# Kernel optimization log

Measured on AMD Instinct MI355X. Metric: run time of the kernel, lower is better.

The kernel has to match this reference:

```python
import jax, jax.numpy as jnp
import numpy as np

BN_EPS = 1e-5

def _bn_eval(x, g, b, m, v):
    # BatchNorm1d in eval mode with running stats
    return (x - m) * (g / jnp.sqrt(v + BN_EPS)) + b

def _gcn_layer(x, adj, w, b):
    # D^-0.5 A D^-0.5 (X W) + b  (same math as diag(d^-0.5) @ adj @ diag(d^-0.5))
    deg = adj.sum(axis=1)
    dis = deg ** -0.5
    xw = x @ w
    return dis[:, None] * (adj @ (dis[:, None] * xw)) + b

def setup_inputs() -> dict:
    key = jax.random.key(0)
    ks = jax.random.split(key, 8)
    N, F, E, H, G, C = 16384, 1024, 256, 256, 128, 10
    def xavier(k, i, o):
        s = float(np.sqrt(6.0 / (i + o)))
        return jax.random.uniform(k, (i, o), jnp.float32, -s, s)
    return {
        "feature": jax.random.uniform(ks[0], (N, F), jnp.float32),
        "adj": jax.random.uniform(ks[1], (N, N), jnp.float32),
        "enc_w1": xavier(ks[2], F, 512), "enc_b1": jnp.zeros((512,), jnp.float32),
        "bn1_g": jnp.ones((512,), jnp.float32), "bn1_b": jnp.zeros((512,), jnp.float32),
        "bn1_m": jnp.zeros((512,), jnp.float32), "bn1_v": jnp.ones((512,), jnp.float32),
        "enc_w2": xavier(ks[3], 512, E), "enc_b2": jnp.zeros((E,), jnp.float32),
        "bn2_g": jnp.ones((E,), jnp.float32), "bn2_b": jnp.zeros((E,), jnp.float32),
        "bn2_m": jnp.zeros((E,), jnp.float32), "bn2_v": jnp.ones((E,), jnp.float32),
        "gcn1_w": xavier(ks[4], E, H), "gcn1_b": jnp.zeros((H,), jnp.float32),
        "gcn2_w": xavier(ks[5], H, G), "gcn2_b": jnp.zeros((G,), jnp.float32),
        "cls_w": xavier(ks[6], G, C), "cls_b": jnp.zeros((C,), jnp.float32),
    }

def reference(feature, adj, enc_w1, enc_b1, bn1_g, bn1_b, bn1_m, bn1_v,
              enc_w2, enc_b2, bn2_g, bn2_b, bn2_m, bn2_v,
              gcn1_w, gcn1_b, gcn2_w, gcn2_b, cls_w, cls_b):
    # encoder.encode (eval: dropout off, BN running stats)
    h = jax.nn.relu(_bn_eval(feature @ enc_w1 + enc_b1, bn1_g, bn1_b, bn1_m, bn1_v))
    h = jax.nn.relu(_bn_eval(h @ enc_w2 + enc_b2, bn2_g, bn2_b, bn2_m, bn2_v))
    h = jax.nn.relu(_gcn_layer(h, adj, gcn1_w, gcn1_b))
    h = jax.nn.relu(_gcn_layer(h, adj, gcn2_w, gcn2_b))
    out = jax.nn.sigmoid(h @ cls_w + cls_b)
    return jnp.clip(out, 1e-10, 1 - 1e-10)
```

## Files before the change

### kernel.cpp

```cpp
#include <hip/hip_runtime.h>
#include <stdint.h>

typedef unsigned short u16;
typedef unsigned int u32;
typedef __attribute__((ext_vector_type(4))) float f32x4;
typedef __attribute__((ext_vector_type(16))) float f32x16;
typedef __attribute__((ext_vector_type(8))) short s16x8;
typedef __attribute__((ext_vector_type(4))) short s16x4;
typedef __attribute__((ext_vector_type(2))) unsigned int u32x2;
typedef __attribute__((ext_vector_type(4))) unsigned int u32x4;
typedef __attribute__((ext_vector_type(8))) int i32x8;

__device__ __forceinline__ u16 f2bf(float x){
  unsigned u = __builtin_bit_cast(unsigned, x);
  u += 0x7fffu + ((u >> 16) & 1u);
  return (u16)(u >> 16);
}
__device__ __forceinline__ float bf2f(u16 b){
  return __builtin_bit_cast(float, (unsigned)b << 16);
}
__device__ __forceinline__ u32 pk_fp8x4(float a, float b, float c, float d){
  int w = 0;
  w = __builtin_amdgcn_cvt_pk_fp8_f32(a, b, w, false);
  w = __builtin_amdgcn_cvt_pk_fp8_f32(c, d, w, true);
  return (u32)w;
}


__device__ __forceinline__ void tcvtT_dev(const float* __restrict__ src, u16* __restrict__ dst,
                                          int K, int N, int bx, int by, char* smem){
  float (*t)[33] = (float (*)[33])smem;
  int tx = threadIdx.x & 31, ty = threadIdx.x >> 5;
  int n0 = bx * 32, k0 = by * 32;
  #pragma unroll
  for (int i = 0; i < 4; i++)
    t[ty + 8 * i][tx] = src[(size_t)(k0 + ty + 8 * i) * N + n0 + tx];
  __syncthreads();
  #pragma unroll
  for (int i = 0; i < 4; i++)
    dst[(size_t)(n0 + ty + 8 * i) * K + k0 + tx] = f2bf(t[tx][ty + 8 * i]);
}

__device__ __forceinline__ void bn_dev(const float* __restrict__ g, const float* __restrict__ b,
                                       const float* __restrict__ m, const float* __restrict__ v,
                                       const float* __restrict__ lin_b,
                                       float* __restrict__ s, float* __restrict__ bb,
                                       int n, int blk){
  int i = blk * 256 + threadIdx.x;
  if (i < n){
    float sc = g[i] * rsqrtf(v[i] + 1e-5f);
    s[i] = sc;
    bb[i] = (lin_b[i] - m[i]) * sc + b[i];
  }
}

__global__ __launch_bounds__(256) void prep0_kernel(
    const float* __restrict__ enc_w1, u16* __restrict__ w1t,
    const float* __restrict__ g, const float* __restrict__ b,
    const float* __restrict__ m, const float* __restrict__ v,
    const float* __restrict__ lin_b, float* __restrict__ s1, float* __restrict__ bb1)
{
  __shared__ char smem[32 * 33 * 4 + 64];
  if (blockIdx.x < 512)
    tcvtT_dev(enc_w1, w1t, 1024, 512, blockIdx.x & 15, blockIdx.x >> 4, smem);
  else
    bn_dev(g, b, m, v, lin_b, s1, bb1, 512, blockIdx.x - 512);
}

__global__ __launch_bounds__(256) void enc1_deg_kernel(
    const float* __restrict__ feature, const u16* __restrict__ w1t,
    u16* __restrict__ h1, const float* __restrict__ cs, const float* __restrict__ cb,
    const float* __restrict__ adj, unsigned char* __restrict__ adj8,
    float* __restrict__ dis,
    const float* __restrict__ enc_w2, u16* __restrict__ w2t,
    const float* __restrict__ gcn1_w, u16* __restrict__ g1t,
    const float* __restrict__ gcn2_w, u16* __restrict__ g2t,
    const float* __restrict__ bn2_g, const float* __restrict__ bn2_b,
    const float* __restrict__ bn2_m, const float* __restrict__ bn2_v,
    const float* __restrict__ enc_b2, float* __restrict__ s2, float* __restrict__ bb2)
{
  constexpr int BM = 128, BN = 256, BK = 64, WM = 2, WN = 2;
  constexpr int N = 512, K = 1024, NADJ = 16384;
  constexpr int WTM = BM / WM, WTN = BN / WN, FM = WTM / 16, FN = WTN / 16;
  constexpr int AIT = (BM * BK) / (256 * 4);
  constexpr int BIT = (BN * BK) / (256 * 8);

  __shared__ __align__(16) char smem[BM * BK * 2 + BN * BK * 2];

  if (blockIdx.x >= 16640){
    int p = blockIdx.x - 16640;
    if (p < 128)       tcvtT_dev(enc_w2, w2t, 512, 256, p & 7, p >> 3, smem);
    else if (p < 192){ int l = p - 128; tcvtT_dev(gcn1_w, g1t, 256, 256, l & 7, l >> 3, smem); }
    else if (p < 224){ int l = p - 192; tcvtT_dev(gcn2_w, g2t, 256, 128, l & 3, l >> 2, smem); }
    else               bn_dev(bn2_g, bn2_b, bn2_m, bn2_v, enc_b2, s2, bb2, 256, 0);
    return;
  }

  if (blockIdx.x >= 256){
    int row = blockIdx.x - 256;
    const float* rp = adj + (size_t)row * NADJ;
    unsigned char* wp = adj8 + (size_t)row * NADJ;
    float s = 0.f;
    #pragma unroll
    for (int it = 0; it < 4; ++it){
      const float* p = rp + it * 4096 + threadIdx.x * 16;
      f32x4 v[4];
      #pragma unroll
      for (int j = 0; j < 4; ++j) v[j] = *(const f32x4*)(p + 4 * j);
      u32x4 o;
      #pragma unroll
      for (int j = 0; j < 4; ++j){
        s += (v[j][0] + v[j][1]) + (v[j][2] + v[j][3]);
        o[j] = pk_fp8x4(v[j][0], v[j][1], v[j][2], v[j][3]);
      }
      *(u32x4*)(wp + it * 4096 + threadIdx.x * 16) = o;
    }
    #pragma unroll
    for (int d = 32; d > 0; d >>= 1) s += __shfl_down(s, d, 64);
    float* ps = (float*)smem;
    if ((threadIdx.x & 63) == 0) ps[threadIdx.x >> 6] = s;
    __syncthreads();
    if (threadIdx.x == 0) dis[row] = rsqrtf((ps[0] + ps[1]) + (ps[2] + ps[3]));
    return;
  }

  u16* As = (u16*)smem;
  u16* Bs = (u16*)(smem + BM * BK * 2);
  const int tid = threadIdx.x;
  const int lane = tid & 63;
  const int wid = tid >> 6;
  const int wr = wid / WN;
  const int wc = wid % WN;
  const int bm = (blockIdx.x & 127) * BM;
  const int bn = (blockIdx.x >> 7) * BN;

  f32x4 arf[AIT];
  s16x8 brb[BIT];

  auto load_tiles = [&](int k0){
    #pragma unroll
    for (int i = 0; i < AIT; i++){
      int e = (i * 256 + tid) * 4; int r = e / BK, c = e % BK;
      arf[i] = *(const f32x4*)(feature + (size_t)(bm + r) * K + k0 + c);
    }
    #pragma unroll
    for (int i = 0; i < BIT; i++){
      int e = (i * 256 + tid) * 8; int r = e / BK, c = e % BK;
      brb[i] = *(const s16x8*)(w1t + (size_t)(bn + r) * K + k0 + c);
    }
  };
  auto store_tiles = [&](){
    char* Ac = (char*)As; char* Bc = (char*)Bs;
    #pragma unroll
    for (int i = 0; i < AIT; i++){
      int e = (i * 256 + tid) * 4; int r = e / BK, c = e % BK;
      int off = ((r * BK + c) * 2) ^ ((r & 7) << 4);
      s16x4 o;
      o[0] = (short)f2bf(arf[i][0]); o[1] = (short)f2bf(arf[i][1]);
      o[2] = (short)f2bf(arf[i][2]); o[3] = (short)f2bf(arf[i][3]);
      *(s16x4*)(Ac + off) = o;
    }
    #pragma unroll
    for (int i = 0; i < BIT; i++){
      int e = (i * 256 + tid) * 8; int r = e / BK, c = e % BK;
      int off = ((r * BK + c) * 2) ^ ((r & 7) << 4);
      *(s16x8*)(Bc + off) = brb[i];
    }
  };

  f32x4 acc[FM][FN];
  #pragma unroll
  for (int m = 0; m < FM; m++)
    #pragma unroll
    for (int n = 0; n < FN; n++)
      acc[m][n] = (f32x4){0.f, 0.f, 0.f, 0.f};

  const int arow0 = wr * WTM + (lane & 15);
  const int brow0 = wc * WTN + (lane & 15);
  const int kof = (lane >> 4) * 8;

  load_tiles(0);
  for (int kt = 0; kt < K / BK; ++kt){
    __syncthreads();
    store_tiles();
    __syncthreads();
    if (kt + 1 < K / BK) load_tiles((kt + 1) * BK);
    const char* Ac = (const char*)As;
    const char* Bc = (const char*)Bs;
    #pragma unroll
    for (int ks = 0; ks < BK / 32; ++ks){
      s16x8 af[FM], bfr[FN];
      #pragma unroll
      for (int m = 0; m < FM; m++){
        int r = arow0 + m * 16;
        af[m] = *(const s16x8*)(Ac + (((r * BK + ks * 32 + kof) * 2) ^ ((r & 7) << 4)));
      }
      #pragma unroll
      for (int n = 0; n < FN; n++){
        int r = brow0 + n * 16;
        bfr[n] = *(const s16x8*)(Bc + (((r * BK + ks * 32 + kof) * 2) ^ ((r & 7) << 4)));
      }
      #pragma unroll
      for (int m = 0; m < FM; m++)
        #pragma unroll
        for (int n = 0; n < FN; n++)
          acc[m][n] = __builtin_amdgcn_mfma_f32_16x16x32_bf16(af[m], bfr[n], acc[m][n], 0, 0, 0);
    }
  }
  #pragma unroll
  for (int m = 0; m < FM; m++){
    #pragma unroll
    for (int n = 0; n < FN; n++){
      int col = bn + wc * WTN + n * 16 + (lane & 15);
      int row0 = bm + wr * WTM + m * 16 + (lane >> 4) * 4;
      #pragma unroll
      for (int r4 = 0; r4 < 4; r4++){
        float vv = fmaxf(acc[m][n][r4] * cs[col] + cb[col], 0.f);
        h1[(size_t)(row0 + r4) * N + col] = f2bf(vv);
      }
    }
  }
}

__global__ __launch_bounds__(256, 1)
void h2tT_kernel(const u16* __restrict__ h1, const u16* __restrict__ w2t,
                 const float* __restrict__ s2, const float* __restrict__ bb2,
                 const u16* __restrict__ g1t, const float* __restrict__ dis,
                 unsigned char* __restrict__ tT)
{
  constexpr int M = 16384, K1 = 512, E = 256, K2 = 256, BK = 64;
  constexpr float SC = 256.f;

  __shared__ u16 As[64 * BK];
  __shared__ u16 Bs[256 * BK];
  __shared__ u16 H2s[64 * 256];

  const int tid = threadIdx.x;
  const int lane = tid & 63;
  const int wc = tid >> 6;
  const int bm = blockIdx.x * 64;
  const int arow0 = lane & 15;
  const int kof = (lane >> 4) * 8;

  {
    s16x8 arb[2], brb[8];
    auto load1 = [&](int k0){
      #pragma unroll
      for (int i = 0; i < 2; i++){
        int e = (i * 256 + tid) * 8; int r = e >> 6, c = e & 63;
        arb[i] = *(const s16x8*)(h1 + (size_t)(bm + r) * K1 + k0 + c);
      }
      #pragma unroll
      for (int i = 0; i < 8; i++){
        int e = (i * 256 + tid) * 8; int r = e >> 6, c = e & 63;
        brb[i] = *(const s16x8*)(w2t + (size_t)r * K1 + k0 + c);
      }
    };
    auto store1 = [&](){
      char* Ac = (char*)As; char* Bc = (char*)Bs;
      #pragma unroll
      for (int i = 0; i < 2; i++){
        int e = (i * 256 + tid) * 8; int r = e >> 6, c = e & 63;
        *(s16x8*)(Ac + (((r * BK + c) * 2) ^ ((r & 7) << 4))) = arb[i];
      }
      #pragma unroll
      for (int i = 0; i < 8; i++){
        int e = (i * 256 + tid) * 8; int r = e >> 6, c = e & 63;
        *(s16x8*)(Bc + (((r * BK + c) * 2) ^ ((r & 7) << 4))) = brb[i];
      }
    };

    f32x4 acc[4][4];
    #pragma unroll
    for (int m = 0; m < 4; m++)
      #pragma unroll
      for (int n = 0; n < 4; n++)
        acc[m][n] = (f32x4){0.f, 0.f, 0.f, 0.f};

    load1(0);
    for (int kt = 0; kt < K1 / BK; ++kt){
      __syncthreads();
      store1();
      __syncthreads();
      if (kt + 1 < K1 / BK) load1((kt + 1) * BK);
      const char* Ac = (const char*)As;
      const char* Bc = (const char*)Bs;
      #pragma unroll
      for (int ks = 0; ks < 2; ++ks){
        s16x8 af[4], bfr[4];
        #pragma unroll
        for (int m = 0; m < 4; m++){
          int r = arow0 + m * 16;
          af[m] = *(const s16x8*)(Ac + (((r * BK + ks * 32 + kof) * 2) ^ ((r & 7) << 4)));
        }
        #pragma unroll
        for (int n = 0; n < 4; n++){
          int r = wc * 64 + n * 16 + (lane & 15);
          bfr[n] = *(const s16x8*)(Bc + (((r * BK + ks * 32 + kof) * 2) ^ ((r & 7) << 4)));
        }
        #pragma unroll
        for (int m = 0; m < 4; m++)
          #pragma unroll
          for (int n = 0; n < 4; n++)
            acc[m][n] = __builtin_amdgcn_mfma_f32_16x16x32_bf16(af[m], bfr[n], acc[m][n], 0, 0, 0);
      }
    }
    __syncthreads();
    char* Hc = (char*)H2s;
    #pragma unroll
    for (int m = 0; m < 4; m++){
      #pragma unroll
      for (int n = 0; n < 4; n++){
        int col = wc * 64 + n * 16 + (lane & 15);
        int row0 = m * 16 + (lane >> 4) * 4;
        #pragma unroll
        for (int r4 = 0; r4 < 4; r4++){
          int row = row0 + r4;
          float vv = fmaxf(acc[m][n][r4] * s2[col] + bb2[col], 0.f);
          *(u16*)(Hc + (((row * 256 + col) * 2) ^ ((row & 7) << 4))) = f2bf(vv);
        }
      }
    }
  }

  {
    s16x8 brb[8];
    auto load2 = [&](int k0){
      #pragma unroll
      for (int i = 0; i < 8; i++){
        int e = (i * 256 + tid) * 8; int r = e >> 6, c = e & 63;
        brb[i] = *(const s16x8*)(g1t + (size_t)r * K2 + k0 + c);
      }
    };
    auto store2 = [&](){
      char* Bc = (char*)Bs;
      #pragma unroll
      for (int i = 0; i < 8; i++){
        int e = (i * 256 + tid) * 8; int r = e >> 6, c = e & 63;
        *(s16x8*)(Bc + (((r * BK + c) * 2) ^ ((r & 7) << 4))) = brb[i];
      }
    };

    f32x4 acc[4][4];
    #pragma unroll
    for (int m = 0; m < 4; m++)
      #pragma unroll
      for (int n = 0; n < 4; n++)
        acc[m][n] = (f32x4){0.f, 0.f, 0.f, 0.f};

    load2(0);
    for (int kt = 0; kt < K2 / BK; ++kt){
      __syncthreads();
      store2();
      __syncthreads();
      if (kt + 1 < K2 / BK) load2((kt + 1) * BK);
      const char* Hc = (const char*)H2s;
      const char* Bc = (const char*)Bs;
      #pragma unroll
      for (int ks = 0; ks < 2; ++ks){
        s16x8 af[4], bfr[4];
        #pragma unroll
        for (int m = 0; m < 4; m++){
          int r = arow0 + m * 16;
          af[m] = *(const s16x8*)(Hc + (((r * 256 + kt * 64 + ks * 32 + kof) * 2) ^ ((r & 7) << 4)));
        }
        #pragma unroll
        for (int n = 0; n < 4; n++){
          int r = wc * 64 + n * 16 + (lane & 15);
          bfr[n] = *(const s16x8*)(Bc + (((r * BK + ks * 32 + kof) * 2) ^ ((r & 7) << 4)));
        }
        #pragma unroll
        for (int m = 0; m < 4; m++)
          #pragma unroll
          for (int n = 0; n < 4; n++)
            acc[m][n] = __builtin_amdgcn_mfma_f32_16x16x32_bf16(af[m], bfr[n], acc[m][n], 0, 0, 0);
      }
    }
    #pragma unroll
    for (int m = 0; m < 4; m++){
      #pragma unroll
      for (int n = 0; n < 4; n++){
        int col = wc * 64 + n * 16 + (lane & 15);
        int row0 = bm + m * 16 + (lane >> 4) * 4;
        float v0 = acc[m][n][0] * dis[row0 + 0] * SC;
        float v1 = acc[m][n][1] * dis[row0 + 1] * SC;
        float v2 = acc[m][n][2] * dis[row0 + 2] * SC;
        float v3 = acc[m][n][3] * dis[row0 + 3] * SC;
        *(u32*)(tT + (size_t)col * M + row0) = pk_fp8x4(v0, v1, v2, v3);
      }
    }
  }
}

template<int BM, int BN>
__global__ __launch_bounds__(512, 1)
void gemm_mx(const unsigned char* __restrict__ A8, const unsigned char* __restrict__ B8,
             float* __restrict__ P, int M, int N, int K, int Ksub)
{
  constexpr int BK = 128;
  constexpr int AT = BM * BK;
  constexpr int BT = BN * BK;
  constexpr int AIT = AT / (512 * 16);
  constexpr int BIT = BT / (512 * 16);
  constexpr int WM = 2, WN = 4;
  constexpr int WTM = BM / WM;
  constexpr int WTN = BN / WN;
  constexpr int FM = WTM / 32;
  constexpr int FN = WTN / 32;
  static_assert(AIT >= 1 && BIT >= 1, "staging");

  __shared__ __align__(16) char LDS[2 * (AT + BT)];

  const int tid = threadIdx.x;
  const int lane = tid & 63;
  const int wid = tid >> 6;
  const int wr = wid >> 2;
  const int wc = wid & 3;
  const int bm = blockIdx.x * BM;
  const int kz = blockIdx.z * Ksub;

  auto stage = [&](int half, int k0){
    char* ab = LDS + half * (AT + BT);
    #pragma unroll
    for (int i = 0; i < AIT; i++){
      int e = (i * 512 + tid) * 16;
      int r = e >> 7, c = e & 127;
      int cc = c ^ ((r & 7) << 4);
      const unsigned char* g = A8 + (size_t)(bm + r) * K + k0 + cc;
      __builtin_amdgcn_global_load_lds((const __attribute__((address_space(1))) unsigned int*)g,
          (__attribute__((address_space(3))) unsigned int*)(ab + e), 16, 0, 0);
    }
    char* bb = ab + AT;
    #pragma unroll
    for (int i = 0; i < BIT; i++){
      int e = (i * 512 + tid) * 16;
      int r = e >> 7, c = e & 127;
      int cc = c ^ ((r & 7) << 4);
      const unsigned char* g = B8 + (size_t)r * K + k0 + cc;
      __builtin_amdgcn_global_load_lds((const __attribute__((address_space(1))) unsigned int*)g,
          (__attribute__((address_space(3))) unsigned int*)(bb + e), 16, 0, 0);
    }
  };

  f32x16 acc[FM][FN];
  #pragma unroll
  for (int m = 0; m < FM; m++)
    #pragma unroll
    for (int n = 0; n < FN; n++)
      #pragma unroll
      for (int i = 0; i < 16; i++)
        acc[m][n][i] = 0.f;

  const int nk = Ksub / BK;
  stage(0, kz);
  for (int kt = 0; kt < nk; ++kt){
    __syncthreads();
    if (kt + 1 < nk) stage((kt + 1) & 1, kz + (kt + 1) * BK);
    const char* ab = LDS + (kt & 1) * (AT + BT);
    const char* bb = ab + AT;
    #pragma unroll
    for (int ks = 0; ks < 2; ks++){
      const int c0 = ks * 64 + (lane >> 5) * 32;
      i32x8 af[FM], bf_[FN];
      #pragma unroll
      for (int m = 0; m < FM; m++){
        int r = wr * WTM + m * 32 + (lane & 31);
        int sw = (r & 7) << 4;
        int o = r * BK + c0;
        u32x4 lo = *(const u32x4*)(ab + (o ^ sw));
        u32x4 hi = *(const u32x4*)(ab + ((o + 16) ^ sw));
        af[m][0] = lo[0]; af[m][1] = lo[1]; af[m][2] = lo[2]; af[m][3] = lo[3];
        af[m][4] = hi[0]; af[m][5] = hi[1]; af[m][6] = hi[2]; af[m][7] = hi[3];
      }
      #pragma unroll
      for (int n = 0; n < FN; n++){
        int r = wc * WTN + n * 32 + (lane & 31);
        int sw = (r & 7) << 4;
        int o = r * BK + c0;
        u32x4 lo = *(const u32x4*)(bb + (o ^ sw));
        u32x4 hi = *(const u32x4*)(bb + ((o + 16) ^ sw));
        bf_[n][0] = lo[0]; bf_[n][1] = lo[1]; bf_[n][2] = lo[2]; bf_[n][3] = lo[3];
        bf_[n][4] = hi[0]; bf_[n][5] = hi[1]; bf_[n][6] = hi[2]; bf_[n][7] = hi[3];
      }
      #pragma unroll
      for (int m = 0; m < FM; m++)
        #pragma unroll
        for (int n = 0; n < FN; n++)
          acc[m][n] = __builtin_amdgcn_mfma_scale_f32_32x32x64_f8f6f4(
              af[m], bf_[n], acc[m][n], 0, 0, 0, 0x7F7F7F7F, 0, 0x7F7F7F7F);
    }
  }

  float* Pz = P + (size_t)blockIdx.z * M * N;
  #pragma unroll
  for (int m = 0; m < FM; m++){
    #pragma unroll
    for (int n = 0; n < FN; n++){
      int colg = wc * WTN + n * 32 + (lane & 31);
      int rbase = bm + wr * WTM + m * 32 + (lane >> 5) * 4;
      #pragma unroll
      for (int i = 0; i < 16; i++){
        int rowg = rbase + (i & 3) + 8 * (i >> 2);
        Pz[(size_t)rowg * N + colg] = acc[m][n][i];
      }
    }
  }
}

__global__ __launch_bounds__(256, 1)
void t2g_kernel(const float* __restrict__ part, const float* __restrict__ dis,
                const float* __restrict__ g1b, const u16* __restrict__ g2t,
                unsigned char* __restrict__ t2T)
{
  constexpr int M = 16384, H = 256, BK = 64;
  constexpr float SC = 256.f, SCI = 1.f / 256.f;
  const size_t MN = (size_t)M * H;

  __shared__ u16 As[64 * BK];
  __shared__ u16 Bs[128 * BK];

  const int tid = threadIdx.x;
  const int lane = tid & 63;
  const int wid = tid >> 6;
  const int wr = wid >> 1;
  const int wc = wid & 1;
  const int bm = blockIdx.x * 64;
  const int kof = (lane >> 4) * 8;

  f32x4 a0r[4], a1r[4], gbr[4];
  float dsr[4];
  s16x8 brb[4];

  auto load_tiles = [&](int k0){
    #pragma unroll
    for (int i = 0; i < 4; i++){
      int e = (i * 256 + tid) * 4; int r = e >> 6, c = e & 63;
      size_t pi = (size_t)(bm + r) * H + k0 + c;
      a0r[i] = *(const f32x4*)(part + pi);
      a1r[i] = *(const f32x4*)(part + MN + pi);
      gbr[i] = *(const f32x4*)(g1b + k0 + c);
      dsr[i] = dis[bm + r];
    }
    #pragma unroll
    for (int i = 0; i < 4; i++){
      int e = (i * 256 + tid) * 8; int r = e >> 6, c = e & 63;
      brb[i] = *(const s16x8*)(g2t + (size_t)r * H + k0 + c);
    }
  };
  auto store_tiles = [&](){
    char* Ac = (char*)As; char* Bc = (char*)Bs;
    #pragma unroll
    for (int i = 0; i < 4; i++){
      int e = (i * 256 + tid) * 4; int r = e >> 6, c = e & 63;
      float dsc = dsr[i] * SCI;
      s16x4 o;
      #pragma unroll
      for (int j = 0; j < 4; j++){
        float vv = fmaxf(dsc * (a0r[i][j] + a1r[i][j]) + gbr[i][j], 0.f);
        o[j] = (short)f2bf(vv);
      }
      *(s16x4*)(Ac + (((r * BK + c) * 2) ^ ((r & 7) << 4))) = o;
    }
    #pragma unroll
    for (int i = 0; i < 4; i++){
      int e = (i * 256 + tid) * 8; int r = e >> 6, c = e & 63;
      *(s16x8*)(Bc + (((r * BK + c) * 2) ^ ((r & 7) << 4))) = brb[i];
    }
  };

  f32x4 acc[2][4];
  #pragma unroll
  for (int m = 0; m < 2; m++)
    #pragma unroll
    for (int n = 0; n < 4; n++)
      acc[m][n] = (f32x4){0.f, 0.f, 0.f, 0.f};

  load_tiles(0);
  for (int kt = 0; kt < H / BK; ++kt){
    __syncthreads();
    store_tiles();
    __syncthreads();
    if (kt + 1 < H / BK) load_tiles((kt + 1) * BK);
    const char* Ac = (const char*)As;
    const char* Bc = (const char*)Bs;
    #pragma unroll
    for (int ks = 0; ks < 2; ++ks){
      s16x8 af[2], bfr[4];
      #pragma unroll
      for (int m = 0; m < 2; m++){
        int r = wr * 32 + m * 16 + (lane & 15);
        af[m] = *(const s16x8*)(Ac + (((r * BK + ks * 32 + kof) * 2) ^ ((r & 7) << 4)));
      }
      #pragma unroll
      for (int n = 0; n < 4; n++){
        int r = wc * 64 + n * 16 + (lane & 15);
        bfr[n] = *(const s16x8*)(Bc + (((r * BK + ks * 32 + kof) * 2) ^ ((r & 7) << 4)));
      }
      #pragma unroll
      for (int m = 0; m < 2; m++)
        #pragma unroll
        for (int n = 0; n < 4; n++)
          acc[m][n] = __builtin_amdgcn_mfma_f32_16x16x32_bf16(af[m], bfr[n], acc[m][n], 0, 0, 0);
    }
  }

  #pragma unroll
  for (int m = 0; m < 2; m++){
    #pragma unroll
    for (int n = 0; n < 4; n++){
      int col = wc * 64 + n * 16 + (lane & 15);
      int row0 = bm + wr * 32 + m * 16 + (lane >> 4) * 4;
      float v0 = acc[m][n][0] * dis[row0 + 0] * SC;
      float v1 = acc[m][n][1] * dis[row0 + 1] * SC;
      float v2 = acc[m][n][2] * dis[row0 + 2] * SC;
      float v3 = acc[m][n][3] * dis[row0 + 3] * SC;
      *(u32*)(t2T + (size_t)col * M + row0) = pk_fp8x4(v0, v1, v2, v3);
    }
  }
}

__global__ __launch_bounds__(256) void cls2_kernel(const float* __restrict__ part,
                                                   const float* __restrict__ dis,
                                                   const float* __restrict__ g2b,
                                                   const float* __restrict__ w,
                                                   const float* __restrict__ b,
                                                   float* __restrict__ out)
{
  constexpr int M = 16384, G = 128;
  constexpr float SCI = 1.f / 256.f;
  const size_t MN = (size_t)M * G;
  __shared__ float ws_[G * 10];
  __shared__ float bs_[10];
  __shared__ float gb_[G];
  for (int i = threadIdx.x; i < G * 10; i += 256) ws_[i] = w[i];
  if (threadIdx.x < 10) bs_[threadIdx.x] = b[threadIdx.x];
  if (threadIdx.x < G) gb_[threadIdx.x] = g2b[threadIdx.x];
  __syncthreads();
  int row = blockIdx.x * 256 + threadIdx.x;
  const float* p0 = part + (size_t)row * G;
  const float* p1 = p0 + MN;
  float dr = dis[row] * SCI;
  float acc[10];
  #pragma unroll
  for (int c = 0; c < 10; c++) acc[c] = bs_[c];
  for (int k16 = 0; k16 < G; k16 += 16){
    f32x4 a0[4], a1[4];
    #pragma unroll
    for (int j = 0; j < 4; j++){
      a0[j] = *(const f32x4*)(p0 + k16 + 4 * j);
      a1[j] = *(const f32x4*)(p1 + k16 + 4 * j);
    }
    #pragma unroll
    for (int j = 0; j < 16; j++){
      float h = fmaxf(dr * (a0[j >> 2][j & 3] + a1[j >> 2][j & 3]) + gb_[k16 + j], 0.f);
      #pragma unroll
      for (int c = 0; c < 10; c++) acc[c] = fmaf(h, ws_[(k16 + j) * 10 + c], acc[c]);
    }
  }
  #pragma unroll
  for (int c = 0; c < 10; c++){
    float sg = 1.f / (1.f + expf(-acc[c]));
    sg = fminf(fmaxf(sg, 1e-10f), 1.f - 1e-10f);
    out[(size_t)row * 10 + c] = sg;
  }
}


extern "C" void kernel_launch(void* const* d_in, const int* in_sizes, int n_in,
                              void* d_out, int out_size, void* d_ws, size_t ws_size,
                              hipStream_t stream)
{
  (void)in_sizes; (void)n_in; (void)out_size; (void)ws_size;
  const float* feature = (const float*)d_in[0];
  const float* adj     = (const float*)d_in[1];
  const float* enc_w1  = (const float*)d_in[2];
  const float* enc_b1  = (const float*)d_in[3];
  const float* bn1_g   = (const float*)d_in[4];
  const float* bn1_b   = (const float*)d_in[5];
  const float* bn1_m   = (const float*)d_in[6];
  const float* bn1_v   = (const float*)d_in[7];
  const float* enc_w2  = (const float*)d_in[8];
  const float* enc_b2  = (const float*)d_in[9];
  const float* bn2_g   = (const float*)d_in[10];
  const float* bn2_b   = (const float*)d_in[11];
  const float* bn2_m   = (const float*)d_in[12];
  const float* bn2_v   = (const float*)d_in[13];
  const float* gcn1_w  = (const float*)d_in[14];
  const float* gcn1_b  = (const float*)d_in[15];
  const float* gcn2_w  = (const float*)d_in[16];
  const float* gcn2_b  = (const float*)d_in[17];
  const float* cls_w   = (const float*)d_in[18];
  const float* cls_b   = (const float*)d_in[19];
  float* out = (float*)d_out;

  const int NN = 16384, F = 1024, H1 = 512, E = 256, H = 256, G = 128;

  char* ws = (char*)d_ws;
  size_t off = 0;
  auto alloc = [&](size_t bytes) -> char* {
    char* p = ws + off; off += (bytes + 255) & ~(size_t)255; return p;
  };
  float* dis = (float*)alloc((size_t)NN * 4);
  float* s1  = (float*)alloc((size_t)H1 * 4);
  float* bb1 = (float*)alloc((size_t)H1 * 4);
  float* s2  = (float*)alloc((size_t)E * 4);
  float* bb2 = (float*)alloc((size_t)E * 4);
  u16* w1t = (u16*)alloc((size_t)H1 * F * 2);
  u16* w2t = (u16*)alloc((size_t)E * H1 * 2);
  u16* g1t = (u16*)alloc((size_t)H * E * 2);
  u16* g2t = (u16*)alloc((size_t)G * H * 2);
  u16* h1  = (u16*)alloc((size_t)NN * H1 * 2);
  unsigned char* tT  = (unsigned char*)alloc((size_t)E * NN);
  unsigned char* t2T = (unsigned char*)alloc((size_t)G * NN);
  float* part = (float*)alloc((size_t)2 * NN * H * 4);
  unsigned char* adj8 = (unsigned char*)alloc((size_t)NN * NN);

  prep0_kernel<<<514, 256, 0, stream>>>(enc_w1, w1t, bn1_g, bn1_b, bn1_m, bn1_v, enc_b1, s1, bb1);

  enc1_deg_kernel<<<256 + NN + 225, 256, 0, stream>>>(
      feature, w1t, h1, s1, bb1, adj, adj8, dis,
      enc_w2, w2t, gcn1_w, g1t, gcn2_w, g2t,
      bn2_g, bn2_b, bn2_m, bn2_v, enc_b2, s2, bb2);

  h2tT_kernel<<<NN / 64, 256, 0, stream>>>(h1, w2t, s2, bb2, g1t, dis, tT);

  gemm_mx<128,256><<<dim3(NN/128, 1, 2), 512, 0, stream>>>(
      adj8, tT, part, NN, H, NN, NN/2);

  t2g_kernel<<<NN / 64, 256, 0, stream>>>(part, dis, gcn1_b, g2t, t2T);

  gemm_mx<128,128><<<dim3(NN/128, 1, 2), 512, 0, stream>>>(
      adj8, t2T, part, NN, G, NN, NN/2);

  cls2_kernel<<<NN / 256, 256, 0, stream>>>(part, dis, gcn2_b, cls_w, cls_b, out);
}
```

Baseline: 494.9 us.

## Stream B operand from global in adjacency GEMM, split K four ways, widen h2tT

The fp8 adjacency GEMM stops staging the B (feature) tile in LDS and reads B fragments straight from global memory (they are small and likely cache-resident), keeping only A double-buffered in LDS. Dropping B from LDS frees shared memory, allowing higher occupancy (launch bounds 512,4). Split-K goes from 2 to 4 slices, so the partial buffer and the downstream reductions in t2g and cls2 now sum four partials. The h2tT kernel is reshaped to 512 threads with 2x4 warps to raise occupancy. The cost is more partial-sum traffic and uncoalesced, latency-exposed global B loads inside the MFMA loop.

New measurement: 606.5 us. 1.23x slower.

```diff
diff --git a/kernel.cpp b/kernel.cpp
--- a/kernel.cpp
+++ b/kernel.cpp
@@ -222,13 +222,13 @@
   }
 }
 
-__global__ __launch_bounds__(256, 1)
+__global__ __launch_bounds__(512, 2)
 void h2tT_kernel(const u16* __restrict__ h1, const u16* __restrict__ w2t,
                  const float* __restrict__ s2, const float* __restrict__ bb2,
                  const u16* __restrict__ g1t, const float* __restrict__ dis,
                  unsigned char* __restrict__ tT)
 {
-  constexpr int M = 16384, K1 = 512, E = 256, K2 = 256, BK = 64;
+  constexpr int M = 16384, K1 = 512, K2 = 256, BK = 64;
   constexpr float SC = 256.f;
 
   __shared__ u16 As[64 * BK];
@@ -237,42 +237,37 @@
 
   const int tid = threadIdx.x;
   const int lane = tid & 63;
-  const int wc = tid >> 6;
+  const int wid = tid >> 6;
+  const int wr = wid >> 2;
+  const int wc = wid & 3;
   const int bm = blockIdx.x * 64;
-  const int arow0 = lane & 15;
   const int kof = (lane >> 4) * 8;
 
   {
-    s16x8 arb[2], brb[8];
+    s16x8 arb, brb[4];
     auto load1 = [&](int k0){
-      #pragma unroll
-      for (int i = 0; i < 2; i++){
-        int e = (i * 256 + tid) * 8; int r = e >> 6, c = e & 63;
-        arb[i] = *(const s16x8*)(h1 + (size_t)(bm + r) * K1 + k0 + c);
-      }
-      #pragma unroll
-      for (int i = 0; i < 8; i++){
-        int e = (i * 256 + tid) * 8; int r = e >> 6, c = e & 63;
+      { int e = tid * 8; int r = e >> 6, c = e & 63;
+        arb = *(const s16x8*)(h1 + (size_t)(bm + r) * K1 + k0 + c); }
+      #pragma unroll
+      for (int i = 0; i < 4; i++){
+        int e = (i * 512 + tid) * 8; int r = e >> 6, c = e & 63;
         brb[i] = *(const s16x8*)(w2t + (size_t)r * K1 + k0 + c);
       }
     };
     auto store1 = [&](){
       char* Ac = (char*)As; char* Bc = (char*)Bs;
-      #pragma unroll
-      for (int i = 0; i < 2; i++){
-        int e = (i * 256 + tid) * 8; int r = e >> 6, c = e & 63;
-        *(s16x8*)(Ac + (((r * BK + c) * 2) ^ ((r & 7) << 4))) = arb[i];
-      }
-      #pragma unroll
-      for (int i = 0; i < 8; i++){
-        int e = (i * 256 + tid) * 8; int r = e >> 6, c = e & 63;
+      { int e = tid * 8; int r = e >> 6, c = e & 63;
+        *(s16x8*)(Ac + (((r * BK + c) * 2) ^ ((r & 7) << 4))) = arb; }
+      #pragma unroll
+      for (int i = 0; i < 4; i++){
+        int e = (i * 512 + tid) * 8; int r = e >> 6, c = e & 63;
         *(s16x8*)(Bc + (((r * BK + c) * 2) ^ ((r & 7) << 4))) = brb[i];
       }
     };
 
-    f32x4 acc[4][4];
-    #pragma unroll
-    for (int m = 0; m < 4; m++)
+    f32x4 acc[2][4];
+    #pragma unroll
+    for (int m = 0; m < 2; m++)
       #pragma unroll
       for (int n = 0; n < 4; n++)
         acc[m][n] = (f32x4){0.f, 0.f, 0.f, 0.f};
@@ -287,10 +282,10 @@
       const char* Bc = (const char*)Bs;
       #pragma unroll
       for (int ks = 0; ks < 2; ++ks){
-        s16x8 af[4], bfr[4];
-        #pragma unroll
-        for (int m = 0; m < 4; m++){
-          int r = arow0 + m * 16;
+        s16x8 af[2], bfr[4];
+        #pragma unroll
+        for (int m = 0; m < 2; m++){
+          int r = wr * 32 + m * 16 + (lane & 15);
           af[m] = *(const s16x8*)(Ac + (((r * BK + ks * 32 + kof) * 2) ^ ((r & 7) << 4)));
         }
         #pragma unroll
@@ -299,7 +294,7 @@
           bfr[n] = *(const s16x8*)(Bc + (((r * BK + ks * 32 + kof) * 2) ^ ((r & 7) << 4)));
         }
         #pragma unroll
-        for (int m = 0; m < 4; m++)
+        for (int m = 0; m < 2; m++)
           #pragma unroll
           for (int n = 0; n < 4; n++)
             acc[m][n] = __builtin_amdgcn_mfma_f32_16x16x32_bf16(af[m], bfr[n], acc[m][n], 0, 0, 0);
@@ -308,11 +303,11 @@
     __syncthreads();
     char* Hc = (char*)H2s;
     #pragma unroll
-    for (int m = 0; m < 4; m++){
+    for (int m = 0; m < 2; m++){
       #pragma unroll
       for (int n = 0; n < 4; n++){
         int col = wc * 64 + n * 16 + (lane & 15);
-        int row0 = m * 16 + (lane >> 4) * 4;
+        int row0 = wr * 32 + m * 16 + (lane >> 4) * 4;
         #pragma unroll
         for (int r4 = 0; r4 < 4; r4++){
           int row = row0 + r4;
@@ -324,26 +319,26 @@
   }
 
   {
-    s16x8 brb[8];
+    s16x8 brb[4];
     auto load2 = [&](int k0){
       #pragma unroll
-      for (int i = 0; i < 8; i++){
-        int e = (i * 256 + tid) * 8; int r = e >> 6, c = e & 63;
+      for (int i = 0; i < 4; i++){
+        int e = (i * 512 + tid) * 8; int r = e >> 6, c = e & 63;
         brb[i] = *(const s16x8*)(g1t + (size_t)r * K2 + k0 + c);
       }
     };
     auto store2 = [&](){
       char* Bc = (char*)Bs;
       #pragma unroll
-      for (int i = 0; i < 8; i++){
-        int e = (i * 256 + tid) * 8; int r = e >> 6, c = e & 63;
+      for (int i = 0; i < 4; i++){
+        int e = (i * 512 + tid) * 8; int r = e >> 6, c = e & 63;
         *(s16x8*)(Bc + (((r * BK + c) * 2) ^ ((r & 7) << 4))) = brb[i];
       }
     };
 
-    f32x4 acc[4][4];
-    #pragma unroll
-    for (int m = 0; m < 4; m++)
+    f32x4 acc[2][4];
+    #pragma unroll
+    for (int m = 0; m < 2; m++)
       #pragma unroll
       for (int n = 0; n < 4; n++)
         acc[m][n] = (f32x4){0.f, 0.f, 0.f, 0.f};
@@ -358,10 +353,10 @@
       const char* Bc = (const char*)Bs;
       #pragma unroll
       for (int ks = 0; ks < 2; ++ks){
-        s16x8 af[4], bfr[4];
-        #pragma unroll
-        for (int m = 0; m < 4; m++){
-          int r = arow0 + m * 16;
+        s16x8 af[2], bfr[4];
+        #pragma unroll
+        for (int m = 0; m < 2; m++){
+          int r = wr * 32 + m * 16 + (lane & 15);
           af[m] = *(const s16x8*)(Hc + (((r * 256 + kt * 64 + ks * 32 + kof) * 2) ^ ((r & 7) << 4)));
         }
         #pragma unroll
@@ -370,18 +365,18 @@
           bfr[n] = *(const s16x8*)(Bc + (((r * BK + ks * 32 + kof) * 2) ^ ((r & 7) << 4)));
         }
         #pragma unroll
-        for (int m = 0; m < 4; m++)
+        for (int m = 0; m < 2; m++)
           #pragma unroll
           for (int n = 0; n < 4; n++)
             acc[m][n] = __builtin_amdgcn_mfma_f32_16x16x32_bf16(af[m], bfr[n], acc[m][n], 0, 0, 0);
       }
     }
     #pragma unroll
-    for (int m = 0; m < 4; m++){
+    for (int m = 0; m < 2; m++){
       #pragma unroll
       for (int n = 0; n < 4; n++){
         int col = wc * 64 + n * 16 + (lane & 15);
-        int row0 = bm + m * 16 + (lane >> 4) * 4;
+        int row0 = bm + wr * 32 + m * 16 + (lane >> 4) * 4;
         float v0 = acc[m][n][0] * dis[row0 + 0] * SC;
         float v1 = acc[m][n][1] * dis[row0 + 1] * SC;
         float v2 = acc[m][n][2] * dis[row0 + 2] * SC;
@@ -392,24 +387,17 @@
   }
 }
 
-template<int BM, int BN>
-__global__ __launch_bounds__(512, 1)
-void gemm_mx(const unsigned char* __restrict__ A8, const unsigned char* __restrict__ B8,
-             float* __restrict__ P, int M, int N, int K, int Ksub)
+template<int BN>
+__global__ __launch_bounds__(512, 4)
+void gemm_mxd(const unsigned char* __restrict__ A8, const unsigned char* __restrict__ B8,
+              float* __restrict__ P, int Ksub)
 {
-  constexpr int BK = 128;
+  constexpr int M = 16384, K = 16384, BM = 128, BK = 128;
   constexpr int AT = BM * BK;
-  constexpr int BT = BN * BK;
-  constexpr int AIT = AT / (512 * 16);
-  constexpr int BIT = BT / (512 * 16);
-  constexpr int WM = 2, WN = 4;
-  constexpr int WTM = BM / WM;
-  constexpr int WTN = BN / WN;
-  constexpr int FM = WTM / 32;
+  constexpr int WTN = BN / 4;
   constexpr int FN = WTN / 32;
-  static_assert(AIT >= 1 && BIT >= 1, "staging");
-
-  __shared__ __align__(16) char LDS[2 * (AT + BT)];
+
+  __shared__ __align__(16) char LDS[2 * AT];
 
   const int tid = threadIdx.x;
   const int lane = tid & 63;
@@ -419,10 +407,10 @@
   const int bm = blockIdx.x * BM;
   const int kz = blockIdx.z * Ksub;
 
-  auto stage = [&](int half, int k0){
-    char* ab = LDS + half * (AT + BT);
-    #pragma unroll
-    for (int i = 0; i < AIT; i++){
+  auto stageA = [&](int half, int k0){
+    char* ab = LDS + half * AT;
+    #pragma unroll
+    for (int i = 0; i < 2; i++){
       int e = (i * 512 + tid) * 16;
       int r = e >> 7, c = e & 127;
       int cc = c ^ ((r & 7) << 4);
@@ -430,21 +418,11 @@
       __builtin_amdgcn_global_load_lds((const __attribute__((address_space(1))) unsigned int*)g,
           (__attribute__((address_space(3))) unsigned int*)(ab + e), 16, 0, 0);
     }
-    char* bb = ab + AT;
-    #pragma unroll
-    for (int i = 0; i < BIT; i++){
-      int e = (i * 512 + tid) * 16;
-      int r = e >> 7, c = e & 127;
-      int cc = c ^ ((r & 7) << 4);
-      const unsigned char* g = B8 + (size_t)r * K + k0 + cc;
-      __builtin_amdgcn_global_load_lds((const __attribute__((address_space(1))) unsigned int*)g,
-          (__attribute__((address_space(3))) unsigned int*)(bb + e), 16, 0, 0);
-    }
   };
 
-  f32x16 acc[FM][FN];
-  #pragma unroll
-  for (int m = 0; m < FM; m++)
+  f32x16 acc[2][FN];
+  #pragma unroll
+  for (int m = 0; m < 2; m++)
     #pragma unroll
     for (int n = 0; n < FN; n++)
       #pragma unroll
@@ -452,56 +430,54 @@
         acc[m][n][i] = 0.f;
 
   const int nk = Ksub / BK;
-  stage(0, kz);
+  stageA(0, kz);
   for (int kt = 0; kt < nk; ++kt){
     __syncthreads();
-    if (kt + 1 < nk) stage((kt + 1) & 1, kz + (kt + 1) * BK);
-    const char* ab = LDS + (kt & 1) * (AT + BT);
-    const char* bb = ab + AT;
+    if (kt + 1 < nk) stageA((kt + 1) & 1, kz + (kt + 1) * BK);
+    const char* ab = LDS + (kt & 1) * AT;
+    const int kb = kz + kt * BK;
     #pragma unroll
     for (int ks = 0; ks < 2; ks++){
       const int c0 = ks * 64 + (lane >> 5) * 32;
-      i32x8 af[FM], bf_[FN];
-      #pragma unroll
-      for (int m = 0; m < FM; m++){
-        int r = wr * WTM + m * 32 + (lane & 31);
+      i32x8 af[2];
+      #pragma unroll
+      for (int m = 0; m < 2; m++){
+        int r = wr * 64 + m * 32 + (lane & 31);
         int sw = (r & 7) << 4;
         int o = r * BK + c0;
         u32x4 lo = *(const u32x4*)(ab + (o ^ sw));
         u32x4 hi = *(const u32x4*)(ab + ((o + 16) ^ sw));
-        af[m][0] = lo[0]; af[m][1] = lo[1]; af[m][2] = lo[2]; af[m][3] = lo[3];
-        af[m][4] = hi[0]; af[m][5] = hi[1]; af[m][6] = hi[2]; af[m][7] = hi[3];
+        af[m][0]=lo[0];af[m][1]=lo[1];af[m][2]=lo[2];af[m][3]=lo[3];
+        af[m][4]=hi[0];af[m][5]=hi[1];af[m][6]=hi[2];af[m][7]=hi[3];
       }
       #pragma unroll
       for (int n = 0; n < FN; n++){
-        int r = wc * WTN + n * 32 + (lane & 31);
-        int sw = (r & 7) << 4;
-        int o = r * BK + c0;
-        u32x4 lo = *(const u32x4*)(bb + (o ^ sw));
-        u32x4 hi = *(const u32x4*)(bb + ((o + 16) ^ sw));
-        bf_[n][0] = lo[0]; bf_[n][1] = lo[1]; bf_[n][2] = lo[2]; bf_[n][3] = lo[3];
-        bf_[n][4] = hi[0]; bf_[n][5] = hi[1]; bf_[n][6] = hi[2]; bf_[n][7] = hi[3];
-      }
-      #pragma unroll
-      for (int m = 0; m < FM; m++)
-        #pragma unroll
-        for (int n = 0; n < FN; n++)
+        int rb = wc * WTN + n * 32 + (lane & 31);
+        const unsigned char* gp = B8 + (size_t)rb * K + kb + c0;
+        u32x4 lo = *(const u32x4*)gp;
+        u32x4 hi = *(const u32x4*)(gp + 16);
+        i32x8 bf;
+        bf[0]=lo[0];bf[1]=lo[1];bf[2]=lo[2];bf[3]=lo[3];
+        bf[4]=hi[0];bf[5]=hi[1];bf[6]=hi[2];bf[7]=hi[3];
+        #pragma unroll
+        for (int m = 0; m < 2; m++)
           acc[m][n] = __builtin_amdgcn_mfma_scale_f32_32x32x64_f8f6f4(
-              af[m], bf_[n], acc[m][n], 0, 0, 0, 0x7F7F7F7F, 0, 0x7F7F7F7F);
-    }
-  }
-
-  float* Pz = P + (size_t)blockIdx.z * M * N;
-  #pragma unroll
-  for (int m = 0; m < FM; m++){
+              af[m], bf, acc[m][n], 0, 0, 0, 0x7F7F7F7F, 0, 0x7F7F7F7F);
+      }
+    }
+  }
+
+  float* Pz = P + (size_t)blockIdx.z * M * BN;
+  #pragma unroll
+  for (int m = 0; m < 2; m++){
     #pragma unroll
     for (int n = 0; n < FN; n++){
       int colg = wc * WTN + n * 32 + (lane & 31);
-      int rbase = bm + wr * WTM + m * 32 + (lane >> 5) * 4;
+      int rbase = bm + wr * 64 + m * 32 + (lane >> 5) * 4;
       #pragma unroll
       for (int i = 0; i < 16; i++){
         int rowg = rbase + (i & 3) + 8 * (i >> 2);
-        Pz[(size_t)rowg * N + colg] = acc[m][n][i];
+        Pz[(size_t)rowg * BN + colg] = acc[m][n][i];
       }
     }
   }
@@ -527,7 +503,7 @@
   const int bm = blockIdx.x * 64;
   const int kof = (lane >> 4) * 8;
 
-  f32x4 a0r[4], a1r[4], gbr[4];
+  f32x4 ar[4][4], gbr[4];
   float dsr[4];
   s16x8 brb[4];
 
@@ -536,8 +512,9 @@
     for (int i = 0; i < 4; i++){
       int e = (i * 256 + tid) * 4; int r = e >> 6, c = e & 63;
       size_t pi = (size_t)(bm + r) * H + k0 + c;
-      a0r[i] = *(const f32x4*)(part + pi);
-      a1r[i] = *(const f32x4*)(part + MN + pi);
+      #pragma unroll
+      for (int s = 0; s < 4; s++)
+        ar[s][i] = *(const f32x4*)(part + s * MN + pi);
       gbr[i] = *(const f32x4*)(g1b + k0 + c);
       dsr[i] = dis[bm + r];
     }
@@ -556,7 +533,7 @@
       s16x4 o;
       #pragma unroll
       for (int j = 0; j < 4; j++){
-        float vv = fmaxf(dsc * (a0r[i][j] + a1r[i][j]) + gbr[i][j], 0.f);
+        float vv = fmaxf(dsc * ((ar[0][i][j] + ar[1][i][j]) + (ar[2][i][j] + ar[3][i][j])) + gbr[i][j], 0.f);
         o[j] = (short)f2bf(vv);
       }
       *(s16x4*)(Ac + (((r * BK + c) * 2) ^ ((r & 7) << 4))) = o;
@@ -638,21 +615,22 @@
   __syncthreads();
   int row = blockIdx.x * 256 + threadIdx.x;
   const float* p0 = part + (size_t)row * G;
-  const float* p1 = p0 + MN;
   float dr = dis[row] * SCI;
   float acc[10];
   #pragma unroll
   for (int c = 0; c < 10; c++) acc[c] = bs_[c];
   for (int k16 = 0; k16 < G; k16 += 16){
-    f32x4 a0[4], a1[4];
+    f32x4 a[4];
     #pragma unroll
     for (int j = 0; j < 4; j++){
-      a0[j] = *(const f32x4*)(p0 + k16 + 4 * j);
-      a1[j] = *(const f32x4*)(p1 + k16 + 4 * j);
+      a[j] = *(const f32x4*)(p0 + k16 + 4 * j);
+      a[j] += *(const f32x4*)(p0 + MN + k16 + 4 * j);
+      a[j] += *(const f32x4*)(p0 + 2 * MN + k16 + 4 * j);
+      a[j] += *(const f32x4*)(p0 + 3 * MN + k16 + 4 * j);
     }
     #pragma unroll
     for (int j = 0; j < 16; j++){
-      float h = fmaxf(dr * (a0[j >> 2][j & 3] + a1[j >> 2][j & 3]) + gb_[k16 + j], 0.f);
+      float h = fmaxf(dr * a[j >> 2][j & 3] + gb_[k16 + j], 0.f);
       #pragma unroll
       for (int c = 0; c < 10; c++) acc[c] = fmaf(h, ws_[(k16 + j) * 10 + c], acc[c]);
     }
@@ -712,7 +690,7 @@
   u16* h1  = (u16*)alloc((size_t)NN * H1 * 2);
   unsigned char* tT  = (unsigned char*)alloc((size_t)E * NN);
   unsigned char* t2T = (unsigned char*)alloc((size_t)G * NN);
-  float* part = (float*)alloc((size_t)2 * NN * H * 4);
+  float* part = (float*)alloc((size_t)4 * NN * H * 4);
   unsigned char* adj8 = (unsigned char*)alloc((size_t)NN * NN);
 
   prep0_kernel<<<514, 256, 0, stream>>>(enc_w1, w1t, bn1_g, bn1_b, bn1_m, bn1_v, enc_b1, s1, bb1);
@@ -722,15 +700,13 @@
       enc_w2, w2t, gcn1_w, g1t, gcn2_w, g2t,
       bn2_g, bn2_b, bn2_m, bn2_v, enc_b2, s2, bb2);
 
-  h2tT_kernel<<<NN / 64, 256, 0, stream>>>(h1, w2t, s2, bb2, g1t, dis, tT);
-
-  gemm_mx<128,256><<<dim3(NN/128, 1, 2), 512, 0, stream>>>(
-      adj8, tT, part, NN, H, NN, NN/2);
+  h2tT_kernel<<<NN / 64, 512, 0, stream>>>(h1, w2t, s2, bb2, g1t, dis, tT);
+
+  gemm_mxd<256><<<dim3(NN/128, 1, 4), 512, 0, stream>>>(adj8, tT, part, NN/4);
 
   t2g_kernel<<<NN / 64, 256, 0, stream>>>(part, dis, gcn1_b, g2t, t2T);
 
-  gemm_mx<128,128><<<dim3(NN/128, 1, 2), 512, 0, stream>>>(
-      adj8, t2T, part, NN, G, NN, NN/2);
+  gemm_mxd<128><<<dim3(NN/128, 1, 4), 512, 0, stream>>>(adj8, t2T, part, NN/4);
 
   cls2_kernel<<<NN / 256, 256, 0, stream>>>(part, dis, gcn2_b, cls_w, cls_b, out);
 }
```
